# Performance work log

Measured on AMD Instinct MI355X. Metric: run time of the kernel, lower is better.

Reference implementation:

```python
import jax, jax.numpy as jnp
import numpy as np

B = 16
H = 56
W = 56
C = 384
NH = 12
HD = C // NH
WS = 7
SHIFT = 3
N = WS * WS
SCALE = HD ** -0.5
EPS = 1e-3  # keras LayerNormalization default epsilon


def _rel_pos_index():
    coords = np.stack(np.meshgrid(np.arange(WS), np.arange(WS), indexing='ij')).reshape(2, -1)
    rel = (coords[:, :, None] - coords[:, None, :]).transpose(1, 2, 0)
    rel[:, :, 0] += WS - 1
    rel[:, :, 1] += WS - 1
    rel[:, :, 0] *= 2 * WS - 1
    return rel.sum(-1)  # [N, N]

REL_IDX = jnp.asarray(_rel_pos_index())


def _shift_mask():
    # faithful reproduction of the TransformerBlock.__init__ mask construction
    mask = np.zeros((1, H, W, 1), np.float32)
    slices = (slice(0, -WS), slice(-WS, -SHIFT), slice(-SHIFT, None))
    cnt = 0
    for hs in slices:
        for ws in slices:
            mask[:, hs, ws, :] = cnt
            cnt += 1
    mw = mask.reshape(1, H // WS, WS, W // WS, WS, 1).transpose(0, 1, 3, 2, 4, 5).reshape(-1, N)
    m = mw[:, None, :] - mw[:, :, None]  # expand_dims(mw,1) - expand_dims(mw,2)
    return np.where(m != 0, np.float32(-100.0), np.float32(0.0))  # [nw, N, N]

MASK = jnp.asarray(_shift_mask())


def _ln(x, g, b):
    mu = x.mean(-1, keepdims=True)
    var = ((x - mu) ** 2).mean(-1, keepdims=True)
    return (x - mu) / jnp.sqrt(var + EPS) * g + b


def _window_partition(x):  # [B,H,W,C] -> [B*nw, N, C]
    b = x.shape[0]
    x = x.reshape(b, H // WS, WS, W // WS, WS, C).transpose(0, 1, 3, 2, 4, 5)
    return x.reshape(-1, N, C)


def _window_reverse(wins, b):  # [B*nw, WS, WS, C] -> [B,H,W,C]
    x = wins.reshape(b, H // WS, W // WS, WS, WS, C).transpose(0, 1, 3, 2, 4, 5)
    return x.reshape(b, H, W, C)


def setup_inputs() -> dict:
    key = jax.random.key(0)
    ks = jax.random.split(key, 8)
    s = 0.02
    return {
        'x': jax.random.normal(ks[0], (B, H * W, C), jnp.float32),
        'ln1_g': jnp.ones((C,), jnp.float32),
        'ln1_b': jnp.zeros((C,), jnp.float32),
        'ln2_g': jnp.ones((C,), jnp.float32),
        'ln2_b': jnp.zeros((C,), jnp.float32),
        'qkv_w': s * jax.random.normal(ks[1], (C, 3 * C), jnp.float32),
        'qkv_b': jnp.zeros((3 * C,), jnp.float32),
        'proj_w': s * jax.random.normal(ks[2], (C, C), jnp.float32),
        'proj_b': jnp.zeros((C,), jnp.float32),
        'mlp_w1': s * jax.random.normal(ks[3], (C, 4 * C), jnp.float32),
        'mlp_b1': jnp.zeros((4 * C,), jnp.float32),
        'mlp_w2': s * jax.random.normal(ks[4], (4 * C, C), jnp.float32),
        'mlp_b2': jnp.zeros((C,), jnp.float32),
        'rel_pos_table': s * jax.random.normal(ks[5], ((2 * WS - 1) * (2 * WS - 1), NH), jnp.float32),
    }


def reference(x, ln1_g, ln1_b, ln2_g, ln2_b, qkv_w, qkv_b, proj_w, proj_b,
              mlp_w1, mlp_b1, mlp_w2, mlp_b2, rel_pos_table):
    skip = x
    y = _ln(x, ln1_g, ln1_b).reshape(B, H, W, C)
    # cyclic shift (faithful to source: shift=(-s, +s))
    y = jnp.roll(y, shift=(-SHIFT, SHIFT), axis=(1, 2))
    wins = _window_partition(y)                      # [nW, N, C]
    nW = wins.shape[0]

    qkv = wins @ qkv_w + qkv_b                       # [nW, N, 3C]
    qkv = qkv.reshape(nW, N, 3, NH, HD).transpose(2, 0, 3, 1, 4)
    q, k, v = qkv[0] * SCALE, qkv[1], qkv[2]         # [nW, NH, N, HD]

    attn = jnp.einsum('whnd,whmd->whnm', q, k)       # [nW, NH, N, N]
    bias = rel_pos_table[REL_IDX.reshape(-1)].reshape(N, N, NH).transpose(2, 0, 1)
    attn = attn + bias[None]

    nw = MASK.shape[0]
    attn = attn.reshape(nW // nw, nw, NH, N, N) + MASK[None, :, None]
    attn = jax.nn.softmax(attn.reshape(nW, NH, N, N), axis=-1)

    out = jnp.einsum('whnm,whmd->wnhd', attn, v).reshape(nW, N, C)
    out = out @ proj_w + proj_b

    y = _window_reverse(out.reshape(-1, WS, WS, C), B)
    # reverse shift (faithful to source: shift=(+s, +s))
    y = jnp.roll(y, shift=(SHIFT, SHIFT), axis=(1, 2))
    x = y.reshape(B, H * W, C) + skip

    skip = x
    y = _ln(x, ln2_g, ln2_b)
    y = jax.nn.gelu(y @ mlp_w1 + mlp_b1, approximate=False)
    y = y @ mlp_w2 + mlp_b2
    return y + skip
```

## Files before the change

kernel.cpp:

```cpp
#include <hip/hip_runtime.h>
#include <hip/hip_bf16.h>
#include <math.h>

typedef __hip_bfloat16 bf16;
typedef unsigned short ushort_t;
typedef __bf16 bf16x8 __attribute__((ext_vector_type(8)));
typedef float f32x4 __attribute__((ext_vector_type(4)));

#define TOKENS 50176
#define CW2 512
#define CROWS2 (CW2 * 49)
#define SCALE_ 0.17677669529663687f

__device__ __forceinline__ float b2f(bf16 v) { return __bfloat162float(v); }
__device__ __forceinline__ bf16  f2b(float v) { return __float2bfloat16(v); }

__global__ __launch_bounds__(256) void wt_bf16(const float* __restrict__ W,
                                               ushort_t* __restrict__ Wt,
                                               int K, int N) {
  int idx = blockIdx.x * 256 + threadIdx.x;
  if (idx >= K * N) return;
  int n = idx / K, k = idx - n * K;
  bf16 h = f2b(W[(size_t)k * N + n]);
  Wt[idx] = *(ushort_t*)&h;
}

__global__ __launch_bounds__(64) void ln1_kernel(const float* __restrict__ x,
                                                 const float* __restrict__ g,
                                                 const float* __restrict__ bta,
                                                 bf16* __restrict__ wins) {
  int t = blockIdx.x;
  int lane = threadIdx.x;
  int w = t / 49, n = t - w * 49;
  int bi = w >> 6, wi = w & 63;
  int hw = wi >> 3, ww = wi & 7;
  int ti = n / 7, tj = n - ti * 7;
  int hr = hw * 7 + ti, wr = ww * 7 + tj;
  int hs = (hr + 3) % 56;
  int wsc = (wr + 53) % 56;
  const float* row = x + ((size_t)bi * 3136 + hs * 56 + wsc) * 384;
  float v[6];
  float s = 0.f, s2 = 0.f;
#pragma unroll
  for (int j = 0; j < 6; ++j) {
    v[j] = row[lane + 64 * j];
    s += v[j]; s2 += v[j] * v[j];
  }
#pragma unroll
  for (int m = 32; m >= 1; m >>= 1) {
    s  += __shfl_xor(s, m, 64);
    s2 += __shfl_xor(s2, m, 64);
  }
  float mu = s * (1.f / 384.f);
  float var = s2 * (1.f / 384.f) - mu * mu;
  float rstd = rsqrtf(var + 1e-3f);
  bf16* orow = wins + (size_t)t * 384;
#pragma unroll
  for (int j = 0; j < 6; ++j) {
    int c = lane + 64 * j;
    orow[c] = f2b((v[j] - mu) * rstd * g[c] + bta[c]);
  }
}

__global__ __launch_bounds__(64) void ln2_kernel(const float* __restrict__ x1,
                                                 const float* __restrict__ g,
                                                 const float* __restrict__ bta,
                                                 bf16* __restrict__ out) {
  int t = blockIdx.x;
  int lane = threadIdx.x;
  const float* row = x1 + (size_t)t * 384;
  float v[6];
  float s = 0.f, s2 = 0.f;
#pragma unroll
  for (int j = 0; j < 6; ++j) {
    v[j] = row[lane + 64 * j];
    s += v[j]; s2 += v[j] * v[j];
  }
#pragma unroll
  for (int m = 32; m >= 1; m >>= 1) {
    s  += __shfl_xor(s, m, 64);
    s2 += __shfl_xor(s2, m, 64);
  }
  float mu = s * (1.f / 384.f);
  float var = s2 * (1.f / 384.f) - mu * mu;
  float rstd = rsqrtf(var + 1e-3f);
  bf16* orow = out + (size_t)t * 384;
#pragma unroll
  for (int j = 0; j < 6; ++j) {
    int c = lane + 64 * j;
    orow[c] = f2b((v[j] - mu) * rstd * g[c] + bta[c]);
  }
}

template<int MODE>
__global__ __launch_bounds__(256) void mfma_gemm(
    const ushort_t* __restrict__ A, const ushort_t* __restrict__ Bt,
    const float* __restrict__ bias, int N, int K,
    const float* __restrict__ resid, void* __restrict__ out_) {
  __shared__ ushort_t As[128 * 72];
  __shared__ ushort_t Bs[128 * 72];
  int tid = threadIdx.x;
  int lane = tid & 63, wv = tid >> 6;
  int wm = wv >> 1, wn = wv & 1;
  int lm = lane & 15, kg = lane >> 4;
  int row0 = blockIdx.x * 128, col0 = blockIdx.y * 128;
  f32x4 acc[4][4];
#pragma unroll
  for (int i = 0; i < 4; ++i)
#pragma unroll
    for (int j = 0; j < 4; ++j) acc[i][j] = (f32x4){0.f, 0.f, 0.f, 0.f};

  for (int k0 = 0; k0 < K; k0 += 64) {
#pragma unroll
    for (int it = 0; it < 4; ++it) {
      int lin = it * 256 + tid;
      int r = lin >> 3, kq = (lin & 7) * 8;
      *(int4*)&As[r * 72 + kq] = *(const int4*)&A[(size_t)(row0 + r) * K + k0 + kq];
      *(int4*)&Bs[r * 72 + kq] = *(const int4*)&Bt[(size_t)(col0 + r) * K + k0 + kq];
    }
    __syncthreads();
#pragma unroll
    for (int kk = 0; kk < 2; ++kk) {
      bf16x8 a[4], b[4];
#pragma unroll
      for (int i = 0; i < 4; ++i) {
        a[i] = *(const bf16x8*)&As[(wm * 64 + i * 16 + lm) * 72 + kk * 32 + kg * 8];
        b[i] = *(const bf16x8*)&Bs[(wn * 64 + i * 16 + lm) * 72 + kk * 32 + kg * 8];
      }
#pragma unroll
      for (int i = 0; i < 4; ++i)
#pragma unroll
        for (int j = 0; j < 4; ++j)
          acc[i][j] = __builtin_amdgcn_mfma_f32_16x16x32_bf16(a[i], b[j], acc[i][j], 0, 0, 0);
    }
    __syncthreads();
  }

  int m0 = row0 + wm * 64, n0 = col0 + wn * 64;
#pragma unroll
  for (int i = 0; i < 4; ++i) {
#pragma unroll
    for (int reg = 0; reg < 4; ++reg) {
      int m = m0 + i * 16 + kg * 4 + reg;
      size_t obase = 0;
      if (MODE == 1) {
        int w = m / 49, nn = m - w * 49;
        int bi = w >> 6, wi = w & 63;
        int hw = wi >> 3, ww = wi & 7;
        int ti = nn / 7, tj = nn - ti * 7;
        int hf = (hw * 7 + ti + 3) % 56, wf = (ww * 7 + tj + 3) % 56;
        obase = ((size_t)bi * 3136 + hf * 56 + wf) * 384;
      }
#pragma unroll
      for (int j = 0; j < 4; ++j) {
        int cN = n0 + j * 16 + lm;
        float v = acc[i][j][reg] + bias[cN];
        if (MODE == 0) {
          ((bf16*)out_)[(size_t)m * N + cN] = f2b(v);
        } else if (MODE == 1) {
          float* O = (float*)out_;
          O[obase + cN] = v + resid[obase + cN];
        } else if (MODE == 2) {
          v = 0.5f * v * (1.f + erff(v * 0.7071067811865475f));
          ((bf16*)out_)[(size_t)m * N + cN] = f2b(v);
        } else {
          float* O = (float*)out_;
          O[(size_t)m * N + cN] = v + resid[(size_t)m * N + cN];
        }
      }
    }
  }
}

__global__ __launch_bounds__(256) void attn_mfma(const ushort_t* __restrict__ qkv_c,
                                                 const float* __restrict__ table,
                                                 ushort_t* __restrict__ attn_c,
                                                 int w_base) {
  int wl = blockIdx.x >> 2, hg = blockIdx.x & 3;
  int w = w_base + wl;
  int wi = w & 63;
  int hw = wi >> 3, ww = wi & 7;
  __shared__ ushort_t Qs[64 * 40];
  __shared__ ushort_t Ks[64 * 40];
  __shared__ ushort_t Vt[32 * 72];
  __shared__ ushort_t Ps[64 * 72];
  __shared__ float bias_s[169 * 12];
  int tid = threadIdx.x;
  int lane = tid & 63, wv = tid >> 6;
  int lm = lane & 15, kg = lane >> 4;

  for (int i = tid; i < 64 * 40; i += 256) { Qs[i] = 0; Ks[i] = 0; }
  for (int i = tid; i < 32 * 72; i += 256) Vt[i] = 0;
  for (int i = tid; i < 169 * 12; i += 256) bias_s[i] = table[i];
  __syncthreads();

  for (int hh = 0; hh < 3; ++hh) {
    int h = hg * 3 + hh;
    const ushort_t* base = qkv_c + (size_t)wl * 49 * 1152 + h * 32;
    for (int idx = tid; idx < 392; idx += 256) {
      int n = idx >> 3, d0 = (idx & 7) * 4;
      const ushort_t* p = base + (size_t)n * 1152 + d0;
      ushort4 q = *(const ushort4*)(p);
      ushort4 k = *(const ushort4*)(p + 384);
      ushort4 v = *(const ushort4*)(p + 768);
      *(ushort4*)&Qs[n * 40 + d0] = q;
      *(ushort4*)&Ks[n * 40 + d0] = k;
      Vt[(d0 + 0) * 72 + n] = v.x;
      Vt[(d0 + 1) * 72 + n] = v.y;
      Vt[(d0 + 2) * 72 + n] = v.z;
      Vt[(d0 + 3) * 72 + n] = v.w;
    }
    __syncthreads();

    bf16x8 qa = *(const bf16x8*)&Qs[(wv * 16 + lm) * 40 + kg * 8];
    f32x4 sacc[4];
#pragma unroll
    for (int jt = 0; jt < 4; ++jt) {
      bf16x8 kb = *(const bf16x8*)&Ks[(jt * 16 + lm) * 40 + kg * 8];
      sacc[jt] = __builtin_amdgcn_mfma_f32_16x16x32_bf16(
          qa, kb, (f32x4){0.f, 0.f, 0.f, 0.f}, 0, 0, 0);
    }

    int i_base = wv * 16 + kg * 4;
#pragma unroll
    for (int reg = 0; reg < 4; ++reg) {
      int i = i_base + reg;
      int ii = (i < 49) ? i : 0;
      int yi = ii / 7, xi = ii - yi * 7;
      int hri = hw * 7 + yi, wri = ww * 7 + xi;
      int ri = (hri < 49 ? 0 : (hri < 53 ? 1 : 2)) * 3 + (wri < 49 ? 0 : (wri < 53 ? 1 : 2));
      float sv[4];
      float mx = -1e30f;
#pragma unroll
      for (int jt = 0; jt < 4; ++jt) {
        int j = jt * 16 + lm;
        int jj = (j < 49) ? j : 0;
        int yj = jj / 7, xj = jj - yj * 7;
        int hrj = hw * 7 + yj, wrj = ww * 7 + xj;
        int rj = (hrj < 49 ? 0 : (hrj < 53 ? 1 : 2)) * 3 + (wrj < 49 ? 0 : (wrj < 53 ? 1 : 2));
        int ridx = (yi - yj + 6) * 13 + (xi - xj + 6);
        float s = sacc[jt][reg] * SCALE_ + bias_s[ridx * 12 + h] + ((ri == rj) ? 0.f : -100.f);
        sv[jt] = (j < 49) ? s : -1e30f;
        mx = fmaxf(mx, sv[jt]);
      }
#pragma unroll
      for (int msk = 1; msk < 16; msk <<= 1) mx = fmaxf(mx, __shfl_xor(mx, msk, 64));
      float sm = 0.f;
#pragma unroll
      for (int jt = 0; jt < 4; ++jt) {
        float e = ((jt * 16 + lm) < 49) ? __expf(sv[jt] - mx) : 0.f;
        sv[jt] = e; sm += e;
      }
#pragma unroll
      for (int msk = 1; msk < 16; msk <<= 1) sm += __shfl_xor(sm, msk, 64);
      float inv = 1.f / sm;
#pragma unroll
      for (int jt = 0; jt < 4; ++jt) {
        bf16 pb = f2b(sv[jt] * inv);
        Ps[(size_t)i * 72 + jt * 16 + lm] = *(ushort_t*)&pb;
      }
    }
    f32x4 oacc[2] = {(f32x4){0.f, 0.f, 0.f, 0.f}, (f32x4){0.f, 0.f, 0.f, 0.f}};
#pragma unroll
    for (int ks = 0; ks < 2; ++ks) {
      bf16x8 pa = *(const bf16x8*)&Ps[(wv * 16 + lm) * 72 + ks * 32 + kg * 8];
#pragma unroll
      for (int dt = 0; dt < 2; ++dt) {
        bf16x8 vb = *(const bf16x8*)&Vt[(dt * 16 + lm) * 72 + ks * 32 + kg * 8];
        oacc[dt] = __builtin_amdgcn_mfma_f32_16x16x32_bf16(pa, vb, oacc[dt], 0, 0, 0);
      }
    }
#pragma unroll
    for (int reg = 0; reg < 4; ++reg) {
      int r = i_base + reg;
      if (r < 49) {
#pragma unroll
        for (int dt = 0; dt < 2; ++dt) {
          bf16 ob = f2b(oacc[dt][reg]);
          attn_c[((size_t)wl * 49 + r) * 384 + h * 32 + dt * 16 + lm] = *(ushort_t*)&ob;
        }
      }
    }
    __syncthreads();
  }
}

extern "C" void kernel_launch(void* const* d_in, const int* in_sizes, int n_in,
                              void* d_out, int out_size, void* d_ws, size_t ws_size,
                              hipStream_t stream) {
  const float* x      = (const float*)d_in[0];
  const float* ln1_g  = (const float*)d_in[1];
  const float* ln1_b  = (const float*)d_in[2];
  const float* ln2_g  = (const float*)d_in[3];
  const float* ln2_b  = (const float*)d_in[4];
  const float* qkv_w  = (const float*)d_in[5];
  const float* qkv_b  = (const float*)d_in[6];
  const float* proj_w = (const float*)d_in[7];
  const float* proj_b = (const float*)d_in[8];
  const float* mlp_w1 = (const float*)d_in[9];
  const float* mlp_b1 = (const float*)d_in[10];
  const float* mlp_w2 = (const float*)d_in[11];
  const float* mlp_b2 = (const float*)d_in[12];
  const float* rel_tb = (const float*)d_in[13];

  char* ws = (char*)d_ws;
  ushort_t* r0 = (ushort_t*)(ws + 0);
  ushort_t* r1 = (ushort_t*)(ws + 38535168ull);
  ushort_t* wq = (ushort_t*)(ws + 115605504ull);
  ushort_t* wp = wq + 442368;
  ushort_t* w1 = wp + 147456;
  ushort_t* w2 = w1 + 589824;
  float* out = (float*)d_out;

  wt_bf16<<<1728, 256, 0, stream>>>(qkv_w, wq, 384, 1152);
  wt_bf16<<<576, 256, 0, stream>>>(proj_w, wp, 384, 384);
  wt_bf16<<<2304, 256, 0, stream>>>(mlp_w1, w1, 384, 1536);
  wt_bf16<<<2304, 256, 0, stream>>>(mlp_w2, w2, 1536, 384);

  ln1_kernel<<<TOKENS, 64, 0, stream>>>(x, ln1_g, ln1_b, (bf16*)r0);

  for (int c = 0; c < 2; ++c) {
    ushort_t* winc = r0 + (size_t)c * CROWS2 * 384;
    mfma_gemm<0><<<dim3(CROWS2 / 128, 9), 256, 0, stream>>>(
        winc, wq, qkv_b, 1152, 384, nullptr, (void*)r1);
    attn_mfma<<<CW2 * 4, 256, 0, stream>>>(r1, rel_tb, winc, c * CW2);
  }

  mfma_gemm<1><<<dim3(TOKENS / 128, 3), 256, 0, stream>>>(
      r0, wp, proj_b, 384, 384, x, (void*)out);

  ln2_kernel<<<TOKENS, 64, 0, stream>>>(out, ln2_g, ln2_b, (bf16*)r0);

  for (int c = 0; c < 2; ++c) {
    ushort_t* lc = r0 + (size_t)c * CROWS2 * 384;
    float* oc = out + (size_t)c * CROWS2 * 384;
    mfma_gemm<2><<<dim3(CROWS2 / 128, 12), 256, 0, stream>>>(
        lc, w1, mlp_b1, 1536, 384, nullptr, (void*)r1);
    mfma_gemm<3><<<dim3(CROWS2 / 128, 3), 256, 0, stream>>>(
        r1, w2, mlp_b2, 384, 1536, oc, (void*)oc);
  }
}
```

Measured before the change: 691.6 us.

## Load GEMM tiles directly to LDS with XOR swizzle and use fast erf GELU

The GEMM tile loads switch from register-staged global-to-LDS copies with a padded layout to direct global_load_lds transfers into an unpadded 64-wide LDS tile. An XOR swizzle on the 16-byte column blocks is meant to avoid bank conflicts, and it also cuts LDS use per block. Separately, the exact erff in the GELU epilogue is replaced by the Abramowitz-Stegun polynomial approximation with __expf, which lowers epilogue arithmetic. The approximation has a max error of about 1e-7 in erf, so accuracy is still acceptable.

```diff
diff --git a/kernel.cpp b/kernel.cpp
--- a/kernel.cpp
+++ b/kernel.cpp
@@ -14,6 +14,17 @@
 
 __device__ __forceinline__ float b2f(bf16 v) { return __bfloat162float(v); }
 __device__ __forceinline__ bf16  f2b(float v) { return __float2bfloat16(v); }
+
+__device__ __forceinline__ float gelu_f(float v) {
+  float x = v * 0.7071067811865475f;
+  float ax = fabsf(x);
+  float t = 1.f / (1.f + 0.3275911f * ax);
+  float poly = ((((1.061405429f * t - 1.453152027f) * t + 1.421413741f) * t
+                 - 0.284496736f) * t + 0.254829592f) * t;
+  float erfv = 1.f - poly * __expf(-ax * ax);
+  erfv = copysignf(erfv, x);
+  return 0.5f * v * (1.f + erfv);
+}
 
 __global__ __launch_bounds__(256) void wt_bf16(const float* __restrict__ W,
                                                ushort_t* __restrict__ Wt,
@@ -97,8 +108,8 @@
     const ushort_t* __restrict__ A, const ushort_t* __restrict__ Bt,
     const float* __restrict__ bias, int N, int K,
     const float* __restrict__ resid, void* __restrict__ out_) {
-  __shared__ ushort_t As[128 * 72];
-  __shared__ ushort_t Bs[128 * 72];
+  __shared__ ushort_t As[128 * 64];
+  __shared__ ushort_t Bs[128 * 64];
   int tid = threadIdx.x;
   int lane = tid & 63, wv = tid >> 6;
   int wm = wv >> 1, wn = wv & 1;
@@ -110,13 +121,23 @@
 #pragma unroll
     for (int j = 0; j < 4; ++j) acc[i][j] = (f32x4){0.f, 0.f, 0.f, 0.f};
 
+  int rsub = lane >> 3;
+  int bblk = lane & 7;
+  int bs = bblk ^ rsub;
+
   for (int k0 = 0; k0 < K; k0 += 64) {
 #pragma unroll
-    for (int it = 0; it < 4; ++it) {
-      int lin = it * 256 + tid;
-      int r = lin >> 3, kq = (lin & 7) * 8;
-      *(int4*)&As[r * 72 + kq] = *(const int4*)&A[(size_t)(row0 + r) * K + k0 + kq];
-      *(int4*)&Bs[r * 72 + kq] = *(const int4*)&Bt[(size_t)(col0 + r) * K + k0 + kq];
+    for (int ch = 0; ch < 4; ++ch) {
+      int r8 = wv * 32 + ch * 8;
+      int r = r8 + rsub;
+      const ushort_t* ga = &A[(size_t)(row0 + r) * K + k0 + bs * 8];
+      const ushort_t* gb = &Bt[(size_t)(col0 + r) * K + k0 + bs * 8];
+      __builtin_amdgcn_global_load_lds(
+          (const __attribute__((address_space(1))) void*)ga,
+          (__attribute__((address_space(3))) void*)&As[r8 * 64], 16, 0, 0);
+      __builtin_amdgcn_global_load_lds(
+          (const __attribute__((address_space(1))) void*)gb,
+          (__attribute__((address_space(3))) void*)&Bs[r8 * 64], 16, 0, 0);
     }
     __syncthreads();
 #pragma unroll
@@ -124,8 +145,10 @@
       bf16x8 a[4], b[4];
 #pragma unroll
       for (int i = 0; i < 4; ++i) {
-        a[i] = *(const bf16x8*)&As[(wm * 64 + i * 16 + lm) * 72 + kk * 32 + kg * 8];
-        b[i] = *(const bf16x8*)&Bs[(wn * 64 + i * 16 + lm) * 72 + kk * 32 + kg * 8];
+        int ra = wm * 64 + i * 16 + lm;
+        int rb = wn * 64 + i * 16 + lm;
+        a[i] = *(const bf16x8*)&As[ra * 64 + (((kk * 4 + kg) ^ (ra & 7)) << 3)];
+        b[i] = *(const bf16x8*)&Bs[rb * 64 + (((kk * 4 + kg) ^ (rb & 7)) << 3)];
       }
 #pragma unroll
       for (int i = 0; i < 4; ++i)
@@ -161,8 +184,7 @@
           float* O = (float*)out_;
           O[obase + cN] = v + resid[obase + cN];
         } else if (MODE == 2) {
-          v = 0.5f * v * (1.f + erff(v * 0.7071067811865475f));
-          ((bf16*)out_)[(size_t)m * N + cN] = f2b(v);
+          ((bf16*)out_)[(size_t)m * N + cN] = f2b(gelu_f(v));
         } else {
           float* O = (float*)out_;
           O[(size_t)m * N + cN] = v + resid[(size_t)m * N + cN];
```

Result: no change. 702.5 us (+1.6%).
